# Performance work log

Measured on AMD Instinct MI355X. Metric: run time of the kernel, lower is better.

Reference implementation:

```python
import jax, jax.numpy as jnp
import numpy as np

N = 8192        # num_node == num_hyperedges
F_DIM = 768
HID = F_DIM // 2
OUT_DIM = 10
NNZ = N * 16
DCAT = F_DIM + 2 * HID


def _lrelu(x, s):
    return jnp.where(x >= 0, x, s * x)


def _graphnorm(x, w, b, ms, eps=1e-5):
    # PyG GraphNorm, single graph: learned mean-centering then RMS over nodes
    mean = jnp.mean(x, axis=0, keepdims=True)
    out = x - ms * mean
    var = jnp.mean(out * out, axis=0, keepdims=True)
    return w * out / jnp.sqrt(var + eps) + b


def _segment_softmax(a, seg, n):
    m = jax.ops.segment_max(a, seg, num_segments=n)
    e = jnp.exp(a - m[seg])
    s = jax.ops.segment_sum(e, seg, num_segments=n)
    return e / (s[seg] + 1e-16)


def _hgconv(x, eattr, row, col, W, att, b):
    # PyG HypergraphConv, heads=1, use_attention=True, attention_mode='node'
    xt = x @ W.T          # [N, F] node lin
    et = eattr @ W.T      # [N_edges, F] hyperedge lin (shared weight)
    alpha = (xt @ att[:F_DIM])[row] + (et @ att[F_DIM:])[col]
    alpha = _lrelu(alpha, 0.2)
    alpha = _segment_softmax(alpha, col, N)  # softmax per hyperedge
    ones = jnp.ones_like(alpha)
    deg_e = jax.ops.segment_sum(ones, col, num_segments=N)
    Bn = jnp.where(deg_e > 0, 1.0 / deg_e, 0.0)
    deg_n = jax.ops.segment_sum(ones, row, num_segments=N)
    Dn = jnp.where(deg_n > 0, 1.0 / deg_n, 0.0)
    # node -> hyperedge
    efeat = jax.ops.segment_sum((Bn[col] * alpha)[:, None] * xt[row], col, num_segments=N)
    # hyperedge -> node
    out = jax.ops.segment_sum((Dn[row] * alpha)[:, None] * efeat[col], row, num_segments=N)
    return out + b


def setup_inputs() -> dict:
    key = jax.random.key(0)
    ks = jax.random.split(key, 16)
    f32 = jnp.float32
    return {
        "x": jax.random.normal(ks[0], (N, F_DIM), dtype=f32),
        "edge_index": jax.random.randint(ks[1], (2, NNZ), 0, N, dtype=jnp.int32),
        "edge_attr": jax.random.normal(ks[2], (N, F_DIM), dtype=f32),
        "gn1_w": jnp.ones((F_DIM,), f32), "gn1_b": jnp.zeros((F_DIM,), f32), "gn1_ms": jnp.ones((F_DIM,), f32),
        "gn2_w": jnp.ones((F_DIM,), f32), "gn2_b": jnp.zeros((F_DIM,), f32), "gn2_ms": jnp.ones((F_DIM,), f32),
        "hg1_W": jax.random.normal(ks[3], (F_DIM, F_DIM), dtype=f32) / np.sqrt(F_DIM),
        "hg1_att": jax.random.normal(ks[4], (2 * F_DIM,), dtype=f32) * 0.05,
        "hg1_b": jnp.zeros((F_DIM,), f32),
        "hg2_W": jax.random.normal(ks[5], (F_DIM, F_DIM), dtype=f32) / np.sqrt(F_DIM),
        "hg2_att": jax.random.normal(ks[6], (2 * F_DIM,), dtype=f32) * 0.05,
        "hg2_b": jnp.zeros((F_DIM,), f32),
        "fc1_W": jax.random.normal(ks[7], (HID, F_DIM), dtype=f32) / np.sqrt(F_DIM),
        "fc1_b": jnp.zeros((HID,), f32),
        "fc2_W": jax.random.normal(ks[8], (HID, F_DIM), dtype=f32) / np.sqrt(F_DIM),
        "fc2_b": jnp.zeros((HID,), f32),
        "attn_W1": jax.random.normal(ks[9], (N, N), dtype=f32) / np.sqrt(N),
        "attn_b1": jnp.zeros((N,), f32),
        "attn_W2": jax.random.normal(ks[10], (N,), dtype=f32) / np.sqrt(N),
        "attn_b2": jnp.zeros((), f32),
        "cls_W": jax.random.normal(ks[11], (OUT_DIM, DCAT), dtype=f32) / np.sqrt(DCAT),
        "cls_b": jnp.zeros((OUT_DIM,), f32),
        "center": jnp.zeros((DCAT,), f32),
    }


def reference(x, edge_index, edge_attr,
              gn1_w, gn1_b, gn1_ms, gn2_w, gn2_b, gn2_ms,
              hg1_W, hg1_att, hg1_b, hg2_W, hg2_att, hg2_b,
              fc1_W, fc1_b, fc2_W, fc2_b,
              attn_W1, attn_b1, attn_W2, attn_b2,
              cls_W, cls_b, center):
    row, col = edge_index[0], edge_index[1]
    h1 = _hgconv(_graphnorm(x, gn1_w, gn1_b, gn1_ms), edge_attr, row, col, hg1_W, hg1_att, hg1_b)
    h1 = _lrelu(h1, 0.01)
    out1 = _lrelu(h1 @ fc1_W.T + fc1_b, 0.01)
    h2 = _hgconv(_graphnorm(h1, gn2_w, gn2_b, gn2_ms), edge_attr, row, col, hg2_W, hg2_att, hg2_b)
    h2 = _lrelu(h2, 0.01)
    out2 = _lrelu(h2 @ fc2_W.T + fc2_b, 0.01)
    cat = jnp.concatenate([x, out1, out2], axis=1)  # [N, DCAT]
    # attention MLP over transposed features: [DCAT, N] -> [DCAT]
    score = jax.nn.relu(cat.T @ attn_W1.T + attn_b1) @ attn_W2 + attn_b2
    score = jax.nn.sigmoid(score) - center
    logits = cat * score[None, :]          # einsum 'ij,j->ij'
    return logits @ cls_W.T + cls_b        # [N, OUT_DIM]
```

## Files before the change

### kernel.cpp

```cpp
#include <hip/hip_runtime.h>
#include <cstddef>

#define NN 8192
#define FD 768
#define HIDD 384
#define NNZE 131072
#define DCATD 1536

typedef short bf16x8 __attribute__((ext_vector_type(8)));
typedef float f32x4 __attribute__((ext_vector_type(4)));

__device__ __forceinline__ short f2bf(float f){
  unsigned u = __float_as_uint(f);
  unsigned r = u + 0x7FFFu + ((u>>16)&1u);
  return (short)(r>>16);
}
__device__ __forceinline__ float bf2f(short s){
  return __uint_as_float(((unsigned)(unsigned short)s)<<16);
}

__device__ __forceinline__ void async_copy16(void* lds, const void* g){
  __builtin_amdgcn_global_load_lds((__attribute__((address_space(1))) void*)g,
                                   (__attribute__((address_space(3))) void*)lds, 16, 0, 0);
}

__global__ void k_hist(const int* __restrict__ row, const int* __restrict__ col,
                       int* __restrict__ cr, int* __restrict__ cc){
  int e = blockIdx.x*256 + threadIdx.x;
  if(e >= NNZE) return;
  atomicAdd(&cc[col[e]], 1);
  atomicAdd(&cr[row[e]], 1);
}

__global__ __launch_bounds__(1024) void k_scan2(const int* __restrict__ cnt_col,
    const int* __restrict__ cnt_row,
    int* __restrict__ col_off, int* __restrict__ row_off,
    int* __restrict__ col_cur, int* __restrict__ row_cur,
    float* __restrict__ Bn, float* __restrict__ Dn){
  const int* cnt = (blockIdx.x==0) ? cnt_col : cnt_row;
  int* offs = (blockIdx.x==0) ? col_off : row_off;
  int* cur  = (blockIdx.x==0) ? col_cur : row_cur;
  float* rec= (blockIdx.x==0) ? Bn : Dn;
  __shared__ int part[1024];
  int t = threadIdx.x;
  int v[8]; int s = 0;
  #pragma unroll
  for(int j=0;j<8;j++){ v[j]=cnt[t*8+j]; s+=v[j]; }
  part[t]=s; __syncthreads();
  for(int d=1; d<1024; d<<=1){
    int mine = part[t];
    int add = (t>=d)? part[t-d] : 0;
    __syncthreads();
    part[t] = mine + add;
    __syncthreads();
  }
  int excl = part[t]-s;
  #pragma unroll
  for(int j=0;j<8;j++){
    offs[t*8+j]=excl; cur[t*8+j]=excl; excl+=v[j];
    rec[t*8+j] = (v[j]>0) ? 1.f/(float)v[j] : 0.f;
  }
  if(t==1023) offs[8192]=excl;
}

__global__ void k_scatter(const int* __restrict__ row, const int* __restrict__ col,
                          int* __restrict__ ccur, int* __restrict__ rcur,
                          int* __restrict__ ceids, int* __restrict__ reids){
  int e = blockIdx.x*256 + threadIdx.x;
  if(e >= NNZE) return;
  int p = atomicAdd(&ccur[col[e]],1); ceids[p]=e;
  int q = atomicAdd(&rcur[row[e]],1); reids[q]=e;
}

__global__ __launch_bounds__(256) void k_cvt_all(int nW1,
    const float* __restrict__ W1, short* __restrict__ W1b,
    const float* __restrict__ hg1W, short* __restrict__ wb1,
    const float* __restrict__ hg2W, short* __restrict__ wb2,
    const float* __restrict__ fc1W, short* __restrict__ fwb1,
    const float* __restrict__ fc2W, short* __restrict__ fwb2){
  int b = blockIdx.x;
  const float* s; short* d; size_t base;
  if(b < nW1){ s=W1; d=W1b; base=(size_t)b*2048; }
  else {
    int r = b - nW1;
    if(r<288){ s=hg1W; d=wb1; base=(size_t)r*2048; }
    else if(r<576){ s=hg2W; d=wb2; base=(size_t)(r-288)*2048; }
    else if(r<720){ s=fc1W; d=fwb1; base=(size_t)(r-576)*2048; }
    else { s=fc2W; d=fwb2; base=(size_t)(r-720)*2048; }
  }
  size_t i = base + (size_t)threadIdx.x*8;
  float4 f0 = *(const float4*)(s+i);
  float4 f1 = *(const float4*)(s+i+4);
  bf16x8 t;
  t[0]=f2bf(f0.x); t[1]=f2bf(f0.y); t[2]=f2bf(f0.z); t[3]=f2bf(f0.w);
  t[4]=f2bf(f1.x); t[5]=f2bf(f1.y); t[6]=f2bf(f1.z); t[7]=f2bf(f1.w);
  *(bf16x8*)(d+i) = t;
}

__global__ __launch_bounds__(256) void k_colstats(const float* __restrict__ src,
                                                  float* __restrict__ gs, float* __restrict__ gss){
  int col = blockIdx.x*256 + threadIdx.x;
  int r0 = blockIdx.y*256;
  float s1=0.f, s2=0.f;
  for(int r=0;r<256;r++){
    float v = src[(size_t)(r0+r)*FD + col];
    s1+=v; s2+=v*v;
  }
  atomicAdd(&gs[col], s1);
  atomicAdd(&gss[col], s2);
}

__global__ __launch_bounds__(256) void k_watt(const float* __restrict__ W, const float* __restrict__ att,
    const float* __restrict__ gs, const float* __restrict__ gss,
    const float* __restrict__ w_, const float* __restrict__ b_, const float* __restrict__ ms_,
    float* __restrict__ gnA, float* __restrict__ gnB,
    float* __restrict__ wxr, float* __restrict__ we){
  int c = blockIdx.x; int t = threadIdx.x;
  float sA=0.f, sB=0.f;
  for(int f=t; f<FD; f+=256){
    float w = W[(size_t)f*FD + c];
    sA += w*att[f];
    sB += w*att[FD+f];
  }
  __shared__ float shA[256], shB[256];
  shA[t]=sA; shB[t]=sB; __syncthreads();
  for(int s=128;s>0;s>>=1){ if(t<s){ shA[t]+=shA[t+s]; shB[t]+=shB[t+s]; } __syncthreads(); }
  if(t==0){
    float mean = gs[c]*(1.f/(float)NN);
    float ex2  = gss[c]*(1.f/(float)NN);
    float ctr  = ms_[c]*mean;
    float var  = ex2 - 2.f*ctr*mean + ctr*ctr;
    float a    = w_[c] / sqrtf(var + 1e-5f);
    gnA[c]=a; gnB[c]=b_[c] - a*ctr;
    wxr[c]=shA[0]; we[c]=shB[0];
  }
}

__global__ __launch_bounds__(64) void k_matvec(const float* __restrict__ src, const float* __restrict__ wv,
    float* __restrict__ out){
  int i = blockIdx.x, l = threadIdx.x;
  float s=0.f;
  for(int c=l;c<FD;c+=64) s += src[(size_t)i*FD+c]*wv[c];
  for(int o=32;o;o>>=1) s += __shfl_down(s,o);
  if(l==0) out[i] = s;
}

__global__ __launch_bounds__(256) void k_affdot(const float* __restrict__ src,
    const float* __restrict__ A, const float* __restrict__ B, const float* __restrict__ wxr,
    short* __restrict__ dstb, float* __restrict__ ax){
  int i = blockIdx.x, t = threadIdx.x;
  float p = 0.f;
  #pragma unroll
  for(int k=0;k<3;k++){
    int c = t + k*256;
    float v = A[c]*src[(size_t)i*FD+c] + B[c];
    dstb[(size_t)i*FD+c] = f2bf(v);
    p += v*wxr[c];
  }
  __shared__ float sh[256];
  sh[t]=p; __syncthreads();
  for(int s=128;s>0;s>>=1){ if(t<s) sh[t]+=sh[t+s]; __syncthreads(); }
  if(t==0) ax[i]=sh[0];
}

__global__ __launch_bounds__(256,6) void gemm_lds(const short* __restrict__ A, const short* __restrict__ B,
    float* __restrict__ C, short* __restrict__ Cb, int M, int N, int K,
    const float* __restrict__ bias, float slope){
  __shared__ __align__(16) short As[2*128*32];
  __shared__ __align__(16) short Bs[2*64*32];
  int t = threadIdx.x;
  int w = t>>6, l = t&63;
  int m0 = blockIdx.y*128, n0 = blockIdx.x*64;
  int wm = w>>1, wn = w&1;
  int li = l&15, q = l>>4;
  const short* Ag = A + (size_t)(m0 + w*16 + (l>>2))*K + (l&3)*8;
  const short* Bg = B + (size_t)(n0 + w*16 + (l>>2))*K + (l&3)*8;
  f32x4 acc[4][2];
  #pragma unroll
  for(int i=0;i<4;i++)
    #pragma unroll
    for(int j=0;j<2;j++) acc[i][j] = (f32x4){0.f,0.f,0.f,0.f};
  for(int k0=0;k0<K;k0+=64){
    #pragma unroll
    for(int kk=0;kk<2;kk++){
      async_copy16(&As[kk*4096 + (w*16)*32],        Ag + k0 + kk*32);
      async_copy16(&As[kk*4096 + (64 + w*16)*32],   Ag + (size_t)64*K + k0 + kk*32);
      async_copy16(&Bs[kk*2048 + (w*16)*32],        Bg + k0 + kk*32);
    }
    __syncthreads();
    #pragma unroll
    for(int kk=0;kk<2;kk++){
      bf16x8 a[4], b[2];
      #pragma unroll
      for(int i=0;i<4;i++) a[i] = *(const bf16x8*)&As[kk*4096 + (wm*64 + i*16 + li)*32 + q*8];
      #pragma unroll
      for(int j=0;j<2;j++) b[j] = *(const bf16x8*)&Bs[kk*2048 + (wn*32 + j*16 + li)*32 + q*8];
      #pragma unroll
      for(int i=0;i<4;i++)
        #pragma unroll
        for(int j=0;j<2;j++)
          acc[i][j] = __builtin_amdgcn_mfma_f32_16x16x32_bf16(a[i], b[j], acc[i][j], 0, 0, 0);
    }
    __syncthreads();
  }
  #pragma unroll
  for(int i=0;i<4;i++){
    int gm = m0 + wm*64 + i*16 + q*4;
    #pragma unroll
    for(int j=0;j<2;j++){
      int gn = n0 + wn*32 + j*16 + li;
      float bv = bias ? bias[gn] : 0.f;
      #pragma unroll
      for(int r=0;r<4;r++){
        float vv = acc[i][j][r] + bv;
        vv = (vv>=0.f) ? vv : vv*slope;
        if(C)  C[(size_t)(gm+r)*N + gn] = vv;
        if(Cb) Cb[(size_t)(gm+r)*N + gn] = f2bf(vv);
      }
    }
  }
}

__global__ __launch_bounds__(256) void k_softmax_seg(const int* __restrict__ offs,
    const int* __restrict__ eids, const int* __restrict__ row,
    const float* __restrict__ ax, const float* __restrict__ ae, float* __restrict__ asm_){
  int seg = blockIdx.x*4 + (threadIdx.x>>6);
  int l = threadIdx.x & 63;
  int beg = offs[seg], end = offs[seg+1];
  if(beg >= end) return;
  float aev = ae[seg];
  float m = -1e30f;
  for(int idx=beg+l; idx<end; idx+=64){
    int e = eids[idx];
    float a = ax[row[e]] + aev; a = (a>=0.f)?a:0.2f*a;
    m = fmaxf(m, a);
  }
  #pragma unroll
  for(int o=1;o<64;o<<=1) m = fmaxf(m, __shfl_xor(m,o));
  float s = 0.f;
  for(int idx=beg+l; idx<end; idx+=64){
    int e = eids[idx];
    float a = ax[row[e]] + aev; a = (a>=0.f)?a:0.2f*a;
    s += expf(a-m);
  }
  #pragma unroll
  for(int o=1;o<64;o<<=1) s += __shfl_xor(s,o);
  float inv = 1.f/(s + 1e-16f);
  for(int idx=beg+l; idx<end; idx+=64){
    int e = eids[idx];
    float a = ax[row[e]] + aev; a = (a>=0.f)?a:0.2f*a;
    asm_[e] = expf(a-m)*inv;
  }
}

__global__ __launch_bounds__(192) void k_seg_gather(const short* __restrict__ srcb,
    const int* __restrict__ offs, const int* __restrict__ eids,
    const int* __restrict__ gidx, const float* __restrict__ alpha_sm,
    const float* __restrict__ segscale, const float* __restrict__ bias, float slope,
    float* __restrict__ dst, short* __restrict__ dstb){
  int c = blockIdx.x, t = threadIdx.x;
  int beg = offs[c], end = offs[c+1];
  float scale = segscale[c];
  __shared__ float wsh[192]; __shared__ int rsh[192];
  float4 acc = {0.f,0.f,0.f,0.f};
  for(int base=beg; base<end; base+=192){
    int idx = base+t;
    if(idx<end){ int e=eids[idx]; wsh[t]=alpha_sm[e]; rsh[t]=gidx[e]; }
    __syncthreads();
    int cnt = min(192, end-base);
    int j=0;
    for(; j+1<cnt; j+=2){
      float w0=wsh[j], w1=wsh[j+1];
      short4 s0 = *((const short4*)(srcb + (size_t)rsh[j]*FD) + t);
      short4 s1 = *((const short4*)(srcb + (size_t)rsh[j+1]*FD) + t);
      acc.x += w0*bf2f(s0.x) + w1*bf2f(s1.x);
      acc.y += w0*bf2f(s0.y) + w1*bf2f(s1.y);
      acc.z += w0*bf2f(s0.z) + w1*bf2f(s1.z);
      acc.w += w0*bf2f(s0.w) + w1*bf2f(s1.w);
    }
    if(j<cnt){
      float w0=wsh[j];
      short4 s0 = *((const short4*)(srcb + (size_t)rsh[j]*FD) + t);
      acc.x += w0*bf2f(s0.x); acc.y += w0*bf2f(s0.y);
      acc.z += w0*bf2f(s0.z); acc.w += w0*bf2f(s0.w);
    }
    __syncthreads();
  }
  acc.x*=scale; acc.y*=scale; acc.z*=scale; acc.w*=scale;
  if(bias){
    float4 bv = *((const float4*)bias + t);
    acc.x+=bv.x; acc.y+=bv.y; acc.z+=bv.z; acc.w+=bv.w;
    acc.x=(acc.x>=0.f)?acc.x:slope*acc.x;
    acc.y=(acc.y>=0.f)?acc.y:slope*acc.y;
    acc.z=(acc.z>=0.f)?acc.z:slope*acc.z;
    acc.w=(acc.w>=0.f)?acc.w:slope*acc.w;
  }
  if(dst) *((float4*)(dst + (size_t)c*FD) + t) = acc;
  if(dstb){
    short4 o; o.x=f2bf(acc.x); o.y=f2bf(acc.y); o.z=f2bf(acc.z); o.w=f2bf(acc.w);
    *((short4*)(dstb + (size_t)c*FD) + t) = o;
  }
}

__global__ __launch_bounds__(256) void k_build_catT(const float* __restrict__ x,
    const float* __restrict__ o1, const float* __restrict__ o2, short* __restrict__ catT){
  __shared__ float tile[32][33];
  int i0 = blockIdx.x*32, d0 = blockIdx.y*32;
  int tx = threadIdx.x, ty = threadIdx.y;
  const float* src; int dof, ld;
  if(d0 < FD){ src=x; dof=d0; ld=FD; }
  else if(d0 < FD+HIDD){ src=o1; dof=d0-FD; ld=HIDD; }
  else { src=o2; dof=d0-FD-HIDD; ld=HIDD; }
  for(int yy=ty; yy<32; yy+=8)
    tile[yy][tx] = src[(size_t)(i0+yy)*ld + dof + tx];
  __syncthreads();
  for(int yy=ty; yy<32; yy+=8)
    catT[(size_t)(d0+yy)*NN + i0 + tx] = f2bf(tile[tx][yy]);
}

__global__ __launch_bounds__(256,6) void attn_gemm_lds(const short* __restrict__ catT,
    const short* __restrict__ W1b, const float* __restrict__ b1, const float* __restrict__ W2,
    float* __restrict__ score_pre){
  const int K = NN;
  __shared__ __align__(16) short As[2*128*32];
  __shared__ __align__(16) short Bs[2*64*32];
  int id = blockIdx.x;
  int cc = id&7, g = id>>3;
  int m_idx = g>>4;
  int n_idx = cc*16 + (g&15);
  int m0 = m_idx*128, n0 = n_idx*64;
  int t = threadIdx.x;
  int w = t>>6, l = t&63;
  int wm = w>>1, wn = w&1;
  int li = l&15, q = l>>4;
  const short* Ag = catT + (size_t)(m0 + w*16 + (l>>2))*K + (l&3)*8;
  const short* Bg = W1b + (size_t)(n0 + w*16 + (l>>2))*K + (l&3)*8;
  f32x4 acc[4][2];
  #pragma unroll
  for(int i=0;i<4;i++)
    #pragma unroll
    for(int j=0;j<2;j++) acc[i][j] = (f32x4){0.f,0.f,0.f,0.f};
  for(int k0=0;k0<K;k0+=64){
    #pragma unroll
    for(int kk=0;kk<2;kk++){
      async_copy16(&As[kk*4096 + (w*16)*32],        Ag + k0 + kk*32);
      async_copy16(&As[kk*4096 + (64 + w*16)*32],   Ag + (size_t)64*K + k0 + kk*32);
      async_copy16(&Bs[kk*2048 + (w*16)*32],        Bg + k0 + kk*32);
    }
    __syncthreads();
    #pragma unroll
    for(int kk=0;kk<2;kk++){
      bf16x8 a[4], b[2];
      #pragma unroll
      for(int i=0;i<4;i++) a[i] = *(const bf16x8*)&As[kk*4096 + (wm*64 + i*16 + li)*32 + q*8];
      #pragma unroll
      for(int j=0;j<2;j++) b[j] = *(const bf16x8*)&Bs[kk*2048 + (wn*32 + j*16 + li)*32 + q*8];
      #pragma unroll
      for(int i=0;i<4;i++)
        #pragma unroll
        for(int j=0;j<2;j++)
          acc[i][j] = __builtin_amdgcn_mfma_f32_16x16x32_bf16(a[i], b[j], acc[i][j], 0, 0, 0);
    }
    __syncthreads();
  }
  float w2v[2], b1v[2];
  #pragma unroll
  for(int j=0;j<2;j++){ int gn = n0 + wn*32 + j*16 + li; w2v[j]=W2[gn]; b1v[j]=b1[gn]; }
  #pragma unroll
  for(int i=0;i<4;i++){
    #pragma unroll
    for(int r=0;r<4;r++){
      float s=0.f;
      #pragma unroll
      for(int j=0;j<2;j++){
        float v = acc[i][j][r] + b1v[j];
        v = v>0.f ? v : 0.f;
        s += v*w2v[j];
      }
      s += __shfl_xor(s,1); s += __shfl_xor(s,2); s += __shfl_xor(s,4); s += __shfl_xor(s,8);
      if(li==0) atomicAdd(&score_pre[m0 + wm*64 + i*16 + q*4 + r], s);
    }
  }
}

__global__ __launch_bounds__(256) void attn_gemm_f32(const short* __restrict__ catT,
    const float* __restrict__ W1, const float* __restrict__ b1, const float* __restrict__ W2,
    float* __restrict__ score_pre){
  const int K = NN;
  int lane = threadIdx.x & 63;
  int wv   = threadIdx.x >> 6;
  int m0 = (blockIdx.x*4 + wv)*64;
  int n0 = blockIdx.y*64;
  int li = lane & 15, q = lane >> 4;
  const short* Ab = catT + (size_t)(m0+li)*K + q*8;
  const float* Bb = W1 + (size_t)(n0+li)*K + q*8;
  f32x4 acc[4][4];
  #pragma unroll
  for(int i=0;i<4;i++)
    #pragma unroll
    for(int j=0;j<4;j++) acc[i][j] = (f32x4){0.f,0.f,0.f,0.f};
  for(int k0=0;k0<K;k0+=32){
    bf16x8 a[4], b[4];
    #pragma unroll
    for(int i=0;i<4;i++) a[i] = *(const bf16x8*)(Ab + (size_t)i*16*K + k0);
    #pragma unroll
    for(int j=0;j<4;j++){
      const float* p = Bb + (size_t)j*16*K + k0;
      float4 f0 = *(const float4*)p;
      float4 f1 = *(const float4*)(p+4);
      bf16x8 t;
      t[0]=f2bf(f0.x); t[1]=f2bf(f0.y); t[2]=f2bf(f0.z); t[3]=f2bf(f0.w);
      t[4]=f2bf(f1.x); t[5]=f2bf(f1.y); t[6]=f2bf(f1.z); t[7]=f2bf(f1.w);
      b[j]=t;
    }
    #pragma unroll
    for(int i=0;i<4;i++)
      #pragma unroll
      for(int j=0;j<4;j++)
        acc[i][j] = __builtin_amdgcn_mfma_f32_16x16x32_bf16(a[i], b[j], acc[i][j], 0, 0, 0);
  }
  float w2v[4], b1v[4];
  #pragma unroll
  for(int j=0;j<4;j++){ int gn=n0+j*16+li; w2v[j]=W2[gn]; b1v[j]=b1[gn]; }
  #pragma unroll
  for(int i=0;i<4;i++){
    #pragma unroll
    for(int r=0;r<4;r++){
      float s=0.f;
      #pragma unroll
      for(int j=0;j<4;j++){
        float v = acc[i][j][r] + b1v[j];
        v = v>0.f ? v : 0.f;
        s += v*w2v[j];
      }
      s += __shfl_xor(s,1); s += __shfl_xor(s,2); s += __shfl_xor(s,4); s += __shfl_xor(s,8);
      if(li==0) atomicAdd(&score_pre[m0 + i*16 + q*4 + r], s);
    }
  }
}

__global__ void k_score(const float* __restrict__ pre, const float* __restrict__ b2,
                        const float* __restrict__ center, const float* __restrict__ clsW,
                        float* __restrict__ sw){
  int d = blockIdx.x*256 + threadIdx.x;
  if(d>=DCATD) return;
  float sc = pre[d] + b2[0];
  sc = 1.f/(1.f+expf(-sc));
  sc -= center[d];
  #pragma unroll
  for(int o=0;o<10;o++) sw[d*10+o] = sc * clsW[(size_t)o*DCATD + d];
}

__global__ __launch_bounds__(64) void k_final(const float* __restrict__ x, const float* __restrict__ o1,
    const float* __restrict__ o2, const float* __restrict__ sw, const float* __restrict__ clsb,
    float* __restrict__ out){
  int i = blockIdx.x, l = threadIdx.x;
  float acc[10];
  #pragma unroll
  for(int o=0;o<10;o++) acc[o]=0.f;
  for(int d=l; d<DCATD; d+=64){
    float v = (d<FD) ? x[(size_t)i*FD + d]
            : (d<FD+HIDD) ? o1[(size_t)i*HIDD + d-FD]
            : o2[(size_t)i*HIDD + d-FD-HIDD];
    const float* s = sw + (size_t)d*10;
    #pragma unroll
    for(int o=0;o<10;o++) acc[o] += v*s[o];
  }
  #pragma unroll
  for(int o=0;o<10;o++){
    float t = acc[o];
    for(int off=32;off;off>>=1) t += __shfl_down(t,off);
    if(l==0) out[(size_t)i*10 + o] = t + clsb[o];
  }
}

extern "C" void kernel_launch(void* const* d_in, const int* in_sizes, int n_in,
                              void* d_out, int out_size, void* d_ws, size_t ws_size,
                              hipStream_t stream) {
  const float* x      = (const float*)d_in[0];
  const int*   ei     = (const int*)d_in[1];
  const float* eattr  = (const float*)d_in[2];
  const float* gn1_w  = (const float*)d_in[3];
  const float* gn1_b  = (const float*)d_in[4];
  const float* gn1_ms = (const float*)d_in[5];
  const float* gn2_w  = (const float*)d_in[6];
  const float* gn2_b  = (const float*)d_in[7];
  const float* gn2_ms = (const float*)d_in[8];
  const float* hg1_W  = (const float*)d_in[9];
  const float* hg1_att= (const float*)d_in[10];
  const float* hg1_b  = (const float*)d_in[11];
  const float* hg2_W  = (const float*)d_in[12];
  const float* hg2_att= (const float*)d_in[13];
  const float* hg2_b  = (const float*)d_in[14];
  const float* fc1_W  = (const float*)d_in[15];
  const float* fc1_b  = (const float*)d_in[16];
  const float* fc2_W  = (const float*)d_in[17];
  const float* fc2_b  = (const float*)d_in[18];
  const float* attn_W1= (const float*)d_in[19];
  const float* attn_b1= (const float*)d_in[20];
  const float* attn_W2= (const float*)d_in[21];
  const float* attn_b2= (const float*)d_in[22];
  const float* cls_W  = (const float*)d_in[23];
  const float* cls_b  = (const float*)d_in[24];
  const float* center = (const float*)d_in[25];
  float* out = (float*)d_out;

  const int* row = ei;
  const int* col = ei + NNZE;

  char* w = (char*)d_ws;
  size_t off = 0;
  auto alloc = [&](size_t bytes)->void*{
    off = (off + 255) & ~(size_t)255;
    void* p = w + off;
    off += bytes;
    return p;
  };
  float* xt    = (float*)alloc((size_t)NN*FD*4);
  float* ef    = (float*)alloc((size_t)NN*FD*4);
  float* h     = (float*)alloc((size_t)NN*FD*4);
  float* out1  = (float*)alloc((size_t)NN*HIDD*4);
  float* out2  = (float*)alloc((size_t)NN*HIDD*4);
  short* inb   = (short*)alloc((size_t)NN*FD*2);
  short* hbf   = (short*)alloc((size_t)NN*FD*2);
  short* wb1   = (short*)alloc((size_t)FD*FD*2);
  short* wb2   = (short*)alloc((size_t)FD*FD*2);
  short* fwb1  = (short*)alloc((size_t)HIDD*FD*2);
  short* fwb2  = (short*)alloc((size_t)HIDD*FD*2);
  int* cnt_col = (int*)alloc(NN*4);
  int* cnt_row = (int*)alloc(NN*4);
  int* col_off = (int*)alloc((NN+1)*4);
  int* row_off = (int*)alloc((NN+1)*4);
  int* col_cur = (int*)alloc(NN*4);
  int* row_cur = (int*)alloc(NN*4);
  int* ceids   = (int*)alloc(NNZE*4);
  int* reids   = (int*)alloc(NNZE*4);
  float* Bn    = (float*)alloc(NN*4);
  float* Dn    = (float*)alloc(NN*4);
  float* a_x   = (float*)alloc(NN*4);
  float* a_e   = (float*)alloc(NN*4);
  float* asm_  = (float*)alloc(NNZE*4);
  float* gsum  = (float*)alloc(FD*4);
  float* gssq  = (float*)alloc(FD*4);
  float* gnA   = (float*)alloc(FD*4);
  float* gnB   = (float*)alloc(FD*4);
  float* wxr   = (float*)alloc(FD*4);
  float* we    = (float*)alloc(FD*4);
  float* score_pre = (float*)alloc(DCATD*4);
  float* sw    = (float*)alloc(DCATD*10*4);
  short* catT  = (short*)ef;
  short* xtb   = (short*)xt;
  short* efb   = (short*)ef;
  size_t off_before_w1b = off;
  short* W1b   = (short*)alloc((size_t)NN*NN*2);
  bool use_w1b = (off <= ws_size);
  if(!use_w1b) off = off_before_w1b;
  (void)n_in; (void)in_sizes; (void)out_size;

  hipMemsetAsync(cnt_col, 0, 2*NN*4, stream);
  k_hist<<<NNZE/256, 256, 0, stream>>>(row, col, cnt_row, cnt_col);
  k_scan2<<<2, 1024, 0, stream>>>(cnt_col, cnt_row, col_off, row_off, col_cur, row_cur, Bn, Dn);
  k_scatter<<<NNZE/256, 256, 0, stream>>>(row, col, col_cur, row_cur, ceids, reids);

  int nW1 = use_w1b ? (int)((size_t)NN*NN/2048) : 0;
  k_cvt_all<<<nW1 + 864, 256, 0, stream>>>(nW1, attn_W1, W1b,
      hg1_W, wb1, hg2_W, wb2, fc1_W, fwb1, fc2_W, fwb2);

  for(int layer=0; layer<2; layer++){
    const float* src_feat = (layer==0) ? x : h;
    const float* gW   = (layer==0) ? gn1_w  : gn2_w;
    const float* gB   = (layer==0) ? gn1_b  : gn2_b;
    const float* gMS  = (layer==0) ? gn1_ms : gn2_ms;
    const float* hgW  = (layer==0) ? hg1_W  : hg2_W;
    const float* hgAtt= (layer==0) ? hg1_att: hg2_att;
    const float* hgB  = (layer==0) ? hg1_b  : hg2_b;
    const short* wbL  = (layer==0) ? wb1    : wb2;
    const short* fwbL = (layer==0) ? fwb1   : fwb2;
    const float* fcB  = (layer==0) ? fc1_b  : fc2_b;
    float* fout       = (layer==0) ? out1   : out2;

    hipMemsetAsync(gsum, 0, 2*FD*4, stream);
    k_colstats<<<dim3(3,32), 256, 0, stream>>>(src_feat, gsum, gssq);
    k_watt<<<FD, 256, 0, stream>>>(hgW, hgAtt, gsum, gssq, gW, gB, gMS, gnA, gnB, wxr, we);
    k_matvec<<<NN, 64, 0, stream>>>(eattr, we, a_e);
    k_affdot<<<NN, 256, 0, stream>>>(src_feat, gnA, gnB, wxr, inb, a_x);
    gemm_lds<<<dim3(FD/64, NN/128), 256, 0, stream>>>(inb, wbL, nullptr, xtb, NN, FD, FD, nullptr, 1.f);
    k_softmax_seg<<<NN/4, 256, 0, stream>>>(col_off, ceids, row, a_x, a_e, asm_);
    k_seg_gather<<<NN, 192, 0, stream>>>(xtb, col_off, ceids, row, asm_, Bn, nullptr, 1.f, nullptr, efb);
    k_seg_gather<<<NN, 192, 0, stream>>>(efb, row_off, reids, col, asm_, Dn, hgB, 0.01f, h, hbf);
    gemm_lds<<<dim3(HIDD/64, NN/128), 256, 0, stream>>>(hbf, fwbL, fout, nullptr, NN, HIDD, FD, fcB, 0.01f);
  }

  k_build_catT<<<dim3(NN/32, DCATD/32), dim3(32,8), 0, stream>>>(x, out1, out2, catT);
  hipMemsetAsync(score_pre, 0, DCATD*4, stream);
  if(use_w1b)
    attn_gemm_lds<<<1536, 256, 0, stream>>>(catT, W1b, attn_b1, attn_W2, score_pre);
  else
    attn_gemm_f32<<<dim3(DCATD/256, NN/64), 256, 0, stream>>>(catT, attn_W1, attn_b1, attn_W2, score_pre);
  k_score<<<DCATD/256, 256, 0, stream>>>(score_pre, attn_b2, center, cls_W, sw);
  k_final<<<NN, 64, 0, stream>>>(x, out1, out2, sw, cls_b, out);
}
```

Measured before the change: 1.218 ms.

## Rewrite attention GEMM as 256x256 tiled 8-wave ping-pong pipeline with swizzled LDS

Replaces the 128x64-tile attention-MLP GEMM with a 256x256-tile, 512-thread kernel using 128KB of dynamic LDS. The kernel double-buffers tiles in LDS, splits each K step into four phases that interleave async global->LDS loads with MFMA work under explicit barriers and s_setprio, and XOR-swizzles the LDS layout to avoid bank conflicts. The aim is to raise data reuse per tile and hide memory latency in the K=8192 reduction. The cost is only 192 blocks on the GPU, which may leave many CUs with just one block each, plus hand-tuned vmcnt waits that are fragile.

```diff
diff --git a/kernel.cpp b/kernel.cpp
--- a/kernel.cpp
+++ b/kernel.cpp
@@ -23,6 +23,8 @@
   __builtin_amdgcn_global_load_lds((__attribute__((address_space(1))) void*)g,
                                    (__attribute__((address_space(3))) void*)lds, 16, 0, 0);
 }
+
+#define SB0() __builtin_amdgcn_sched_barrier(0)
 
 __global__ void k_hist(const int* __restrict__ row, const int* __restrict__ col,
                        int* __restrict__ cr, int* __restrict__ cc){
@@ -318,67 +320,146 @@
     catT[(size_t)(d0+yy)*NN + i0 + tx] = f2bf(tile[tx][yy]);
 }
 
-__global__ __launch_bounds__(256,6) void attn_gemm_lds(const short* __restrict__ catT,
+
+__device__ __forceinline__ bf16x8 lds_frag(const short* buf, int r, int cq){
+  int ch = (r*8 + cq) ^ (r&7);
+  return *(const bf16x8*)(buf + ch*8);
+}
+
+__device__ __forceinline__ void stage_half(const short* __restrict__ src, int grow0, int K,
+    short* ldsbuf, int half, int k0, int w, int l, int q_src){
+  #pragma unroll
+  for(int inst=0; inst<2; inst++){
+    int r_local = half*128 + w*16 + inst*8;
+    const short* g = src + (size_t)(grow0 + r_local + (l>>3))*K + k0 + q_src*8;
+    async_copy16(ldsbuf + r_local*64, g);
+  }
+}
+
+__device__ __forceinline__ void read_aquad(bf16x8 (&a)[4][2], const short* Ab, int rbase, int li, int qq){
+  #pragma unroll
+  for(int ii=0; ii<4; ii++)
+    #pragma unroll
+    for(int ks=0; ks<2; ks++)
+      a[ii][ks] = lds_frag(Ab, rbase + ii*32 + li, ks*4 + qq);
+}
+__device__ __forceinline__ void read_bpair(bf16x8 (&b)[2][2], const short* Bb, int rbase, int li, int qq){
+  #pragma unroll
+  for(int jj=0; jj<2; jj++)
+    #pragma unroll
+    for(int ks=0; ks<2; ks++)
+      b[jj][ks] = lds_frag(Bb, rbase + jj*64 + li, ks*4 + qq);
+}
+template<int QM, int QN>
+__device__ __forceinline__ void mfma_quad(f32x4 (&acc)[8][4], const bf16x8 (&a)[4][2], const bf16x8 (&b)[2][2]){
+  #pragma unroll
+  for(int ii=0; ii<4; ii++)
+    #pragma unroll
+    for(int jj=0; jj<2; jj++)
+      #pragma unroll
+      for(int ks=0; ks<2; ks++)
+        acc[QM*4+ii][QN*2+jj] =
+          __builtin_amdgcn_mfma_f32_16x16x32_bf16(a[ii][ks], b[jj][ks], acc[QM*4+ii][QN*2+jj], 0, 0, 0);
+}
+
+#define PHASE_MID() do{ SB0(); asm volatile("s_waitcnt vmcnt(4)" ::: "memory"); SB0(); \
+                        __builtin_amdgcn_s_barrier(); SB0(); }while(0)
+#define LGKM0()     do{ asm volatile("s_waitcnt lgkmcnt(0)" ::: "memory"); SB0(); }while(0)
+#define PHASE_END() do{ SB0(); __builtin_amdgcn_s_barrier(); SB0(); }while(0)
+
+__global__ __launch_bounds__(512,2) void attn_gemm_8ph(const short* __restrict__ catT,
     const short* __restrict__ W1b, const float* __restrict__ b1, const float* __restrict__ W2,
     float* __restrict__ score_pre){
+  extern __shared__ short lds[];
+  short* AsB = lds;
+  short* BsB = lds + 2*256*64;
   const int K = NN;
-  __shared__ __align__(16) short As[2*128*32];
-  __shared__ __align__(16) short Bs[2*64*32];
+  const int nkt = K/64;
   int id = blockIdx.x;
   int cc = id&7, g = id>>3;
-  int m_idx = g>>4;
-  int n_idx = cc*16 + (g&15);
-  int m0 = m_idx*128, n0 = n_idx*64;
-  int t = threadIdx.x;
-  int w = t>>6, l = t&63;
-  int wm = w>>1, wn = w&1;
-  int li = l&15, q = l>>4;
-  const short* Ag = catT + (size_t)(m0 + w*16 + (l>>2))*K + (l&3)*8;
-  const short* Bg = W1b + (size_t)(n0 + w*16 + (l>>2))*K + (l&3)*8;
-  f32x4 acc[4][2];
-  #pragma unroll
-  for(int i=0;i<4;i++)
-    #pragma unroll
-    for(int j=0;j<2;j++) acc[i][j] = (f32x4){0.f,0.f,0.f,0.f};
-  for(int k0=0;k0<K;k0+=64){
-    #pragma unroll
-    for(int kk=0;kk<2;kk++){
-      async_copy16(&As[kk*4096 + (w*16)*32],        Ag + k0 + kk*32);
-      async_copy16(&As[kk*4096 + (64 + w*16)*32],   Ag + (size_t)64*K + k0 + kk*32);
-      async_copy16(&Bs[kk*2048 + (w*16)*32],        Bg + k0 + kk*32);
-    }
-    __syncthreads();
-    #pragma unroll
-    for(int kk=0;kk<2;kk++){
-      bf16x8 a[4], b[2];
-      #pragma unroll
-      for(int i=0;i<4;i++) a[i] = *(const bf16x8*)&As[kk*4096 + (wm*64 + i*16 + li)*32 + q*8];
-      #pragma unroll
-      for(int j=0;j<2;j++) b[j] = *(const bf16x8*)&Bs[kk*2048 + (wn*32 + j*16 + li)*32 + q*8];
-      #pragma unroll
-      for(int i=0;i<4;i++)
-        #pragma unroll
-        for(int j=0;j<2;j++)
-          acc[i][j] = __builtin_amdgcn_mfma_f32_16x16x32_bf16(a[i], b[j], acc[i][j], 0, 0, 0);
-    }
-    __syncthreads();
-  }
-  float w2v[2], b1v[2];
-  #pragma unroll
-  for(int j=0;j<2;j++){ int gn = n0 + wn*32 + j*16 + li; w2v[j]=W2[gn]; b1v[j]=b1[gn]; }
-  #pragma unroll
-  for(int i=0;i<4;i++){
-    #pragma unroll
-    for(int r=0;r<4;r++){
+  int m0 = (g%6)*256;
+  int n0 = (cc*4 + g/6)*256;
+  int tid = threadIdx.x;
+  int w = tid>>6, l = tid&63;
+  int wm = w>>2, wn = w&3;
+  int li = l&15, qq = l>>4;
+  int q_src = (l&7) ^ (l>>3);
+
+  f32x4 acc[8][4];
+  #pragma unroll
+  for(int i=0;i<8;i++)
+    #pragma unroll
+    for(int j=0;j<4;j++) acc[i][j] = (f32x4){0.f,0.f,0.f,0.f};
+
+  stage_half(catT, m0, K, AsB, 0, 0, w, l, q_src);
+  stage_half(catT, m0, K, AsB, 1, 0, w, l, q_src);
+  stage_half(W1b,  n0, K, BsB, 0, 0, w, l, q_src);
+  stage_half(W1b,  n0, K, BsB, 1, 0, w, l, q_src);
+  SB0();
+  asm volatile("s_waitcnt vmcnt(0)" ::: "memory");
+  SB0();
+  __builtin_amdgcn_s_barrier();
+  SB0();
+
+  bf16x8 a[4][2], b0[2][2], b1f[2][2];
+  #pragma unroll 1
+  for(int t=0; t<nkt; ++t){
+    short* Ab = AsB + (t&1)*16384;
+    short* Bb = BsB + (t&1)*16384;
+    short* An = AsB + ((t&1)^1)*16384;
+    short* Bn = BsB + ((t&1)^1)*16384;
+    int k1 = (t+1)*64;
+    bool pf = (t+1 < nkt);
+    read_aquad(a,  Ab, wm*16,        li, qq);
+    read_bpair(b0, Bb, wn*16,        li, qq);
+    if(pf) stage_half(catT, m0, K, An, 0, k1, w, l, q_src);
+    else { SB0(); asm volatile("s_waitcnt vmcnt(0)" ::: "memory"); SB0(); }
+    PHASE_MID();
+    LGKM0();
+    __builtin_amdgcn_s_setprio(1);
+    mfma_quad<0,0>(acc, a, b0);
+    __builtin_amdgcn_s_setprio(0);
+    PHASE_END();
+    read_bpair(b1f, Bb, 128 + wn*16, li, qq);
+    if(pf) stage_half(W1b, n0, K, Bn, 0, k1, w, l, q_src);
+    PHASE_MID();
+    LGKM0();
+    __builtin_amdgcn_s_setprio(1);
+    mfma_quad<0,1>(acc, a, b1f);
+    __builtin_amdgcn_s_setprio(0);
+    PHASE_END();
+    read_aquad(a, Ab, 128 + wm*16,   li, qq);
+    if(pf) stage_half(W1b, n0, K, Bn, 1, k1, w, l, q_src);
+    PHASE_MID();
+    LGKM0();
+    __builtin_amdgcn_s_setprio(1);
+    mfma_quad<1,1>(acc, a, b1f);
+    __builtin_amdgcn_s_setprio(0);
+    PHASE_END();
+    if(pf) stage_half(catT, m0, K, An, 1, k1, w, l, q_src);
+    PHASE_MID();
+    __builtin_amdgcn_s_setprio(1);
+    mfma_quad<1,0>(acc, a, b0);
+    __builtin_amdgcn_s_setprio(0);
+    PHASE_END();
+  }
+
+  float w2v[4], b1v[4];
+  #pragma unroll
+  for(int j=0;j<4;j++){ int gn = n0 + j*64 + wn*16 + li; w2v[j]=W2[gn]; b1v[j]=b1[gn]; }
+  #pragma unroll
+  for(int i=0;i<8;i++){
+    #pragma unroll
+    for(int rr=0;rr<4;rr++){
       float s=0.f;
       #pragma unroll
-      for(int j=0;j<2;j++){
-        float v = acc[i][j][r] + b1v[j];
+      for(int j=0;j<4;j++){
+        float v = acc[i][j][rr] + b1v[j];
         v = v>0.f ? v : 0.f;
         s += v*w2v[j];
       }
       s += __shfl_xor(s,1); s += __shfl_xor(s,2); s += __shfl_xor(s,4); s += __shfl_xor(s,8);
-      if(li==0) atomicAdd(&score_pre[m0 + wm*64 + i*16 + q*4 + r], s);
+      if(li==0) atomicAdd(&score_pre[m0 + i*32 + wm*16 + qq*4 + rr], s);
     }
   }
 }
@@ -593,10 +674,17 @@
 
   k_build_catT<<<dim3(NN/32, DCATD/32), dim3(32,8), 0, stream>>>(x, out1, out2, catT);
   hipMemsetAsync(score_pre, 0, DCATD*4, stream);
-  if(use_w1b)
-    attn_gemm_lds<<<1536, 256, 0, stream>>>(catT, W1b, attn_b1, attn_W2, score_pre);
-  else
+  if(use_w1b){
+    static bool attr_set = false;
+    if(!attr_set){
+      hipFuncSetAttribute(reinterpret_cast<const void*>(attn_gemm_8ph),
+                          hipFuncAttributeMaxDynamicSharedMemorySize, 131072);
+      attr_set = true;
+    }
+    attn_gemm_8ph<<<192, 512, 131072, stream>>>(catT, W1b, attn_b1, attn_W2, score_pre);
+  } else {
     attn_gemm_f32<<<dim3(DCATD/256, NN/64), 256, 0, stream>>>(catT, attn_W1, attn_b1, attn_W2, score_pre);
+  }
   k_score<<<DCATD/256, 256, 0, stream>>>(score_pre, attn_b2, center, cls_W, sw);
   k_final<<<NN, 64, 0, stream>>>(x, out1, out2, sw, cls_b, out);
 }
```

New measurement: 1.087 ms. 1.12x faster.
